# Kernel optimization log

Hardware: AMD Instinct MI355X
Metric: run time of the kernel (lower is better)

## Reference

```python
import jax, jax.numpy as jnp
import numpy as np

EDGE_TEXT_IMG = 2
D_MODEL = 256
N_HEADS = 8
N_LAYERS = 3
INPUT_DIM = 768
LN_EPS = 1e-5
CONFLICT_EPS = 1e-6


def setup_inputs() -> dict:
    key = jax.random.key(0)
    ks = jax.random.split(key, 32)
    B, N, E = 16, 512, 4096
    d, H, L = D_MODEL, N_HEADS, N_LAYERS
    s = 0.02
    inp = {
        'node_feats': jax.random.normal(ks[0], (B, N, INPUT_DIM), jnp.float32),
        'node_mask': jnp.ones((B, N), bool),
        'text_mask': jax.random.randint(ks[1], (B, N), 0, 2).astype(bool),
        'image_mask': jax.random.randint(ks[2], (B, N), 0, 2).astype(bool),
        'global_indices': jax.random.randint(ks[3], (B,), 0, N),
        'edge_index': jax.random.randint(ks[4], (B, 2, E), 0, N),
        'edge_type': jax.random.randint(ks[5], (B, E), 0, 4),
        'edge_weight': jax.random.uniform(ks[6], (B, E), jnp.float32),
        # params
        'W_in': jax.random.normal(ks[7], (INPUT_DIM, d)) * s,
        'b_in': jnp.zeros((d,)),
        'Wqkv': jax.random.normal(ks[8], (L, d, 3 * d)) * s,
        'bqkv': jnp.zeros((L, 3 * d)),
        'Wo': jax.random.normal(ks[9], (L, d, d)) * s,
        'bo': jnp.zeros((L, d)),
        'ln1_g': jnp.ones((L, d)), 'ln1_b': jnp.zeros((L, d)),
        'ln2_g': jnp.ones((L, d)), 'ln2_b': jnp.zeros((L, d)),
        'Wff1': jax.random.normal(ks[10], (L, d, 4 * d)) * s,
        'bff1': jnp.zeros((L, 4 * d)),
        'Wff2': jax.random.normal(ks[11], (L, 4 * d, d)) * s,
        'bff2': jnp.zeros((L, d)),
        'et_emb': jax.random.normal(ks[12], (4, H)) * s,
        'Wm1': jax.random.normal(ks[13], (3 * d + 1, 2 * d)) * s,
        'bm1': jnp.zeros((2 * d,)),
        'Wm2': jax.random.normal(ks[14], (2 * d, d)) * s,
        'bm2': jnp.zeros((d,)),
        'Wm3': jax.random.normal(ks[15], (d, 1)) * s,
        'bm3': jnp.zeros((1,)),
    }
    return inp


def _ln(x, g, b):
    mu = jnp.mean(x, -1, keepdims=True)
    var = jnp.mean((x - mu) ** 2, -1, keepdims=True)
    return (x - mu) * jax.lax.rsqrt(var + LN_EPS) * g + b


def _build_bias(edge_index, edge_type, edge_weight, et_emb, N):
    # vectorized scatter-add of per-edge head biases into dense [B,H,N,N]
    B = edge_index.shape[0]
    src, dst = edge_index[:, 0], edge_index[:, 1]  # [B,E]
    vals = et_emb[edge_type]  # [B,E,H]
    vals = vals + jnp.where(edge_type == EDGE_TEXT_IMG, edge_weight, 0.0)[..., None]
    bias = jnp.zeros((B, N, N, et_emb.shape[1]), vals.dtype)
    bias = bias.at[jnp.arange(B)[:, None], src, dst].add(vals)
    return bias.transpose(0, 3, 1, 2)  # [B,H,N,N]


def _forward(node_feats, node_mask, text_mask, image_mask, global_indices,
             edge_index, edge_type, edge_weight,
             W_in, b_in, Wqkv, bqkv, Wo, bo, ln1_g, ln1_b, ln2_g, ln2_b,
             Wff1, bff1, Wff2, bff2, et_emb, Wm1, bm1, Wm2, bm2, Wm3, bm3):
    B, N, _ = node_feats.shape
    H = N_HEADS
    hd = D_MODEL // H
    attn_bias = _build_bias(edge_index, edge_type, edge_weight, et_emb, N)
    x = node_feats @ W_in + b_in  # [B,N,d]
    key_mask = node_mask[:, None, None, :]  # [B,1,1,N]
    for l in range(N_LAYERS):
        qkv = x @ Wqkv[l] + bqkv[l]
        qkv = qkv.reshape(B, N, 3, H, hd).transpose(2, 0, 3, 1, 4)
        q, k, v = qkv[0], qkv[1], qkv[2]  # [B,H,N,hd]
        scores = jnp.einsum('bhnd,bhmd->bhnm', q, k) / np.sqrt(hd).astype(np.float32)
        scores = scores + attn_bias
        scores = jnp.where(key_mask, scores, -jnp.inf)
        attn = jax.nn.softmax(scores, axis=-1)
        out = jnp.einsum('bhnm,bhmd->bhnd', attn, v)
        out = out.transpose(0, 2, 1, 3).reshape(B, N, D_MODEL)
        out = out @ Wo[l] + bo[l]
        x = _ln(x + out, ln1_g[l], ln1_b[l])
        ff = jax.nn.gelu(x @ Wff1[l] + bff1[l], approximate=False) @ Wff2[l] + bff2[l]
        x = _ln(x + ff, ln2_g[l], ln2_b[l])
    tm = text_mask.astype(x.dtype)
    im = image_mask.astype(x.dtype)
    tc = jnp.clip(tm.sum(1, keepdims=True), 1.0)
    ic = jnp.clip(im.sum(1, keepdims=True), 1.0)
    text_pool = (x * tm[..., None]).sum(1) / tc
    image_pool = (x * im[..., None]).sum(1) / ic
    global_embeds = x[jnp.arange(B), global_indices]
    n1 = jnp.maximum(jnp.linalg.norm(text_pool, axis=-1), CONFLICT_EPS)
    n2 = jnp.maximum(jnp.linalg.norm(image_pool, axis=-1), CONFLICT_EPS)
    cos = jnp.sum(text_pool * image_pool, -1) / (n1 * n2)
    conflict = (1.0 - cos)[:, None]
    combined = jnp.concatenate([global_embeds, text_pool, image_pool, conflict], -1)
    h = jax.nn.gelu(combined @ Wm1 + bm1, approximate=False)
    h = jax.nn.gelu(h @ Wm2 + bm2, approximate=False)
    logits = (h @ Wm3 + bm3)[:, 0]
    return logits


def reference(node_feats, node_mask, text_mask, image_mask, global_indices,
              edge_index, edge_type, edge_weight,
              W_in, b_in, Wqkv, bqkv, Wo, bo, ln1_g, ln1_b, ln2_g, ln2_b,
              Wff1, bff1, Wff2, bff2, et_emb, Wm1, bm1, Wm2, bm2, Wm3, bm3):
    return _forward(node_feats, node_mask, text_mask, image_mask, global_indices,
                    edge_index, edge_type, edge_weight,
                    W_in, b_in, Wqkv, bqkv, Wo, bo, ln1_g, ln1_b, ln2_g, ln2_b,
                    Wff1, bff1, Wff2, bff2, et_emb, Wm1, bm1, Wm2, bm2, Wm3, bm3)
```

## Files before the change

kernel.cpp:

```cpp
#include <hip/hip_runtime.h>
#include <hip/hip_bf16.h>
#include <math.h>

#define Bb 16
#define Nn 512
#define Dd 256
#define Hh 8
#define HD 32
#define Ll 3
#define INDIM 768
#define Ee 4096
#define FF 1024
#define KP 40
#define NBUCK 32768

typedef unsigned short u16;
typedef __bf16 bf16x8 __attribute__((ext_vector_type(8)));
typedef float f32x4 __attribute__((ext_vector_type(4)));
typedef u16 us8 __attribute__((ext_vector_type(8)));
typedef u16 us4 __attribute__((ext_vector_type(4)));

__device__ __forceinline__ float gelu_exact(float x) {
    return 0.5f * x * (1.0f + erff(x * 0.70710678118654752f));
}

__device__ __forceinline__ u16 f2bf(float x) {
    unsigned int u = __float_as_uint(x);
    return (u16)((u + 0x7FFFu + ((u >> 16) & 1u)) >> 16);
}
__device__ __forceinline__ float bf2f(u16 h) {
    return __uint_as_float(((unsigned int)h) << 16);
}

__device__ __forceinline__ int ebucket(int b, int src, int dst) {
    return ((b * 32 + (src >> 4)) * 4 + (dst >> 7)) * 16 + (src & 15);
}


__global__ __launch_bounds__(256) void zero_kernel(int* __restrict__ p, int n) {
    int gid = blockIdx.x * 256 + threadIdx.x;
    if (gid < n) p[gid] = 0;
}

__global__ __launch_bounds__(256) void count_kernel(const int* __restrict__ edge_index,
                                                    int* __restrict__ counts) {
    int gid = blockIdx.x * 256 + threadIdx.x;
    int b = gid >> 12;
    int e = gid & (Ee - 1);
    int src = edge_index[b * 2 * Ee + e];
    int dst = edge_index[b * 2 * Ee + Ee + e];
    atomicAdd(&counts[ebucket(b, src, dst)], 1);
}

__global__ __launch_bounds__(1024) void scan_kernel(const int* __restrict__ counts,
                                                    int* __restrict__ offsets,
                                                    int* __restrict__ cursor) {
    __shared__ int ssum[1024];
    int t = threadIdx.x;
    int local[32];
    int s = 0;
#pragma unroll
    for (int i = 0; i < 32; i++) { local[i] = counts[t * 32 + i]; s += local[i]; }
    ssum[t] = s;
    __syncthreads();
    for (int off = 1; off < 1024; off *= 2) {
        __syncthreads();
        int v = (t >= off) ? ssum[t - off] : 0;
        __syncthreads();
        ssum[t] += v;
    }
    __syncthreads();
    int base = (t > 0) ? ssum[t - 1] : 0;
#pragma unroll
    for (int i = 0; i < 32; i++) {
        offsets[t * 32 + i] = base;
        cursor[t * 32 + i] = base;
        base += local[i];
    }
    if (t == 1023) offsets[NBUCK] = base;
}

__global__ __launch_bounds__(256) void scatter_kernel(const int* __restrict__ edge_index,
                                                      const int* __restrict__ edge_type,
                                                      const float* __restrict__ edge_weight,
                                                      int* __restrict__ cursor,
                                                      int2* __restrict__ pelist) {
    int gid = blockIdx.x * 256 + threadIdx.x;
    int b = gid >> 12;
    int e = gid & (Ee - 1);
    int src = edge_index[b * 2 * Ee + e];
    int dst = edge_index[b * 2 * Ee + Ee + e];
    int ty = edge_type[b * Ee + e];
    float wgt = edge_weight[b * Ee + e];
    int pos = atomicAdd(&cursor[ebucket(b, src, dst)], 1);
    int2 pe;
    pe.x = (src << 20) | (dst << 4) | ty;
    pe.y = __float_as_int(wgt);
    pelist[pos] = pe;
}


__global__ __launch_bounds__(256) void wsplit(const float* __restrict__ W,
                                              u16* __restrict__ Wh,
                                              u16* __restrict__ Wl,
                                              int K, int N) {
    size_t moff = (size_t)blockIdx.z * K * N;
    const float* Ws = W + moff;
    u16* Whs = Wh + moff;
    u16* Wls = Wl + moff;
    int n = blockIdx.x * 256 + threadIdx.x;
    int k0 = blockIdx.y * 8;
    float w[8];
#pragma unroll
    for (int i = 0; i < 8; i++) w[i] = Ws[(size_t)(k0 + i) * N + n];
    u16 h[8], l[8];
#pragma unroll
    for (int i = 0; i < 8; i++) {
        h[i] = f2bf(w[i]);
        l[i] = f2bf(w[i] - bf2f(h[i]));
    }
    us8 hv = {h[0], h[1], h[2], h[3], h[4], h[5], h[6], h[7]};
    us8 lv = {l[0], l[1], l[2], l[3], l[4], l[5], l[6], l[7]};
    *(us8*)&Whs[(size_t)n * K + k0] = hv;
    *(us8*)&Wls[(size_t)n * K + k0] = lv;
}


__global__ __launch_bounds__(256) void gemm_mfma64(const float* __restrict__ A,
                                                   const u16* __restrict__ Bh,
                                                   const u16* __restrict__ Bl,
                                                   const float* __restrict__ bias,
                                                   float* __restrict__ C,
                                                   int M, int K, int N, int act) {
    __shared__ u16 sAh[64 * KP];
    __shared__ u16 sAl[64 * KP];
    __shared__ u16 sBh[64 * KP];
    __shared__ u16 sBl[64 * KP];

    int t = threadIdx.x;
    int w = t >> 6, L = t & 63;
    int wr = w >> 1, wc = w & 1;
    int lane15 = L & 15, quad = L >> 4;
    int row0 = blockIdx.y * 64, col0 = blockIdx.x * 64;

    f32x4 acc[2][2];
#pragma unroll
    for (int mi = 0; mi < 2; mi++)
#pragma unroll
        for (int ni = 0; ni < 2; ni++) acc[mi][ni] = {0.f, 0.f, 0.f, 0.f};

    int ar0 = t >> 3, akq0 = (t & 7) * 4;
    int bn0 = t >> 2, bk0 = (t & 3) * 8;

    const float* Ap0 = &A[(size_t)(row0 + ar0) * K + akq0];
    const float* Ap1 = &A[(size_t)(row0 + ar0 + 32) * K + akq0];
    const u16* Bhp = &Bh[(size_t)(col0 + bn0) * K + bk0];
    const u16* Blp = &Bl[(size_t)(col0 + bn0) * K + bk0];

    float4 av0 = *(const float4*)&Ap0[0];
    float4 av1 = *(const float4*)&Ap1[0];
    us8 bhv = *(const us8*)&Bhp[0];
    us8 blv = *(const us8*)&Blp[0];

    for (int k0 = 0; k0 < K; k0 += 32) {
        __syncthreads();
        {
            float a[4] = {av0.x, av0.y, av0.z, av0.w};
            u16 h[4], l[4];
#pragma unroll
            for (int i = 0; i < 4; i++) { h[i] = f2bf(a[i]); l[i] = f2bf(a[i] - bf2f(h[i])); }
            us4 hv = {h[0], h[1], h[2], h[3]};
            us4 lv = {l[0], l[1], l[2], l[3]};
            *(us4*)&sAh[ar0 * KP + akq0] = hv;
            *(us4*)&sAl[ar0 * KP + akq0] = lv;
        }
        {
            float a[4] = {av1.x, av1.y, av1.z, av1.w};
            u16 h[4], l[4];
#pragma unroll
            for (int i = 0; i < 4; i++) { h[i] = f2bf(a[i]); l[i] = f2bf(a[i] - bf2f(h[i])); }
            us4 hv = {h[0], h[1], h[2], h[3]};
            us4 lv = {l[0], l[1], l[2], l[3]};
            *(us4*)&sAh[(ar0 + 32) * KP + akq0] = hv;
            *(us4*)&sAl[(ar0 + 32) * KP + akq0] = lv;
        }
        *(us8*)&sBh[bn0 * KP + bk0] = bhv;
        *(us8*)&sBl[bn0 * KP + bk0] = blv;
        __syncthreads();

        if (k0 + 32 < K) {
            av0 = *(const float4*)&Ap0[k0 + 32];
            av1 = *(const float4*)&Ap1[k0 + 32];
            bhv = *(const us8*)&Bhp[k0 + 32];
            blv = *(const us8*)&Blp[k0 + 32];
        }

        us8 ahr[2], alr[2], bhr[2], blr[2];
#pragma unroll
        for (int mi = 0; mi < 2; mi++) {
            int ro = (wr * 32 + mi * 16 + lane15) * KP + quad * 8;
            ahr[mi] = *(const us8*)&sAh[ro];
            alr[mi] = *(const us8*)&sAl[ro];
        }
#pragma unroll
        for (int ni = 0; ni < 2; ni++) {
            int ro = (wc * 32 + ni * 16 + lane15) * KP + quad * 8;
            bhr[ni] = *(const us8*)&sBh[ro];
            blr[ni] = *(const us8*)&sBl[ro];
        }
#pragma unroll
        for (int mi = 0; mi < 2; mi++) {
            bf16x8 ah = *(const bf16x8*)&ahr[mi];
            bf16x8 al = *(const bf16x8*)&alr[mi];
#pragma unroll
            for (int ni = 0; ni < 2; ni++) {
                bf16x8 bh = *(const bf16x8*)&bhr[ni];
                bf16x8 bl = *(const bf16x8*)&blr[ni];
                acc[mi][ni] = __builtin_amdgcn_mfma_f32_16x16x32_bf16(ah, bh, acc[mi][ni], 0, 0, 0);
                acc[mi][ni] = __builtin_amdgcn_mfma_f32_16x16x32_bf16(ah, bl, acc[mi][ni], 0, 0, 0);
                acc[mi][ni] = __builtin_amdgcn_mfma_f32_16x16x32_bf16(al, bh, acc[mi][ni], 0, 0, 0);
            }
        }
    }

#pragma unroll
    for (int mi = 0; mi < 2; mi++) {
#pragma unroll
        for (int ni = 0; ni < 2; ni++) {
            int col = col0 + wc * 32 + ni * 16 + lane15;
            float bcol = bias[col];
#pragma unroll
            for (int r = 0; r < 4; r++) {
                int row = row0 + wr * 32 + mi * 16 + quad * 4 + r;
                float u = acc[mi][ni][r] + bcol;
                if (act == 1) u = gelu_exact(u);
                C[(size_t)row * N + col] = u;
            }
        }
    }
}


__global__ __launch_bounds__(256) void gemm_mfma128(const float* __restrict__ A,
                                                    const u16* __restrict__ Bh,
                                                    const u16* __restrict__ Bl,
                                                    const float* __restrict__ bias,
                                                    float* __restrict__ C,
                                                    int M, int K, int N, int act) {
    __shared__ u16 sAh[128 * KP];
    __shared__ u16 sAl[128 * KP];
    __shared__ u16 sBh[128 * KP];
    __shared__ u16 sBl[128 * KP];

    int t = threadIdx.x;
    int w = t >> 6, L = t & 63;
    int wr = w >> 1, wc = w & 1;
    int lane15 = L & 15, quad = L >> 4;
    int row0 = blockIdx.y * 128, col0 = blockIdx.x * 128;

    f32x4 acc[4][4];
#pragma unroll
    for (int mi = 0; mi < 4; mi++)
#pragma unroll
        for (int ni = 0; ni < 4; ni++) acc[mi][ni] = {0.f, 0.f, 0.f, 0.f};

    int ar0 = t >> 3, ak0 = (t & 7) * 4;
    int bn0 = t >> 2, bk0 = (t & 3) * 8;

    const float* Ap = &A[(size_t)(row0 + ar0) * K + ak0];
    const u16* Bhp = &Bh[(size_t)(col0 + bn0) * K + bk0];
    const u16* Blp = &Bl[(size_t)(col0 + bn0) * K + bk0];

    float4 av[4];
    us8 bhv[2], blv[2];
#pragma unroll
    for (int i = 0; i < 4; i++) av[i] = *(const float4*)&Ap[(size_t)(32 * i) * K];
#pragma unroll
    for (int i = 0; i < 2; i++) {
        bhv[i] = *(const us8*)&Bhp[(size_t)(64 * i) * K];
        blv[i] = *(const us8*)&Blp[(size_t)(64 * i) * K];
    }

    for (int k0 = 0; k0 < K; k0 += 32) {
        __syncthreads();
#pragma unroll
        for (int i = 0; i < 4; i++) {
            float a[4] = {av[i].x, av[i].y, av[i].z, av[i].w};
            u16 h[4], l[4];
#pragma unroll
            for (int j = 0; j < 4; j++) { h[j] = f2bf(a[j]); l[j] = f2bf(a[j] - bf2f(h[j])); }
            us4 hv = {h[0], h[1], h[2], h[3]};
            us4 lv = {l[0], l[1], l[2], l[3]};
            *(us4*)&sAh[(ar0 + 32 * i) * KP + ak0] = hv;
            *(us4*)&sAl[(ar0 + 32 * i) * KP + ak0] = lv;
        }
#pragma unroll
        for (int i = 0; i < 2; i++) {
            *(us8*)&sBh[(bn0 + 64 * i) * KP + bk0] = bhv[i];
            *(us8*)&sBl[(bn0 + 64 * i) * KP + bk0] = blv[i];
        }
        __syncthreads();

        if (k0 + 32 < K) {
#pragma unroll
            for (int i = 0; i < 4; i++) av[i] = *(const float4*)&Ap[(size_t)(32 * i) * K + k0 + 32];
#pragma unroll
            for (int i = 0; i < 2; i++) {
                bhv[i] = *(const us8*)&Bhp[(size_t)(64 * i) * K + k0 + 32];
                blv[i] = *(const us8*)&Blp[(size_t)(64 * i) * K + k0 + 32];
            }
        }

        us8 ahr[4], alr[4], bhr[4], blr[4];
#pragma unroll
        for (int mi = 0; mi < 4; mi++) {
            int ro = (wr * 64 + mi * 16 + lane15) * KP + quad * 8;
            ahr[mi] = *(const us8*)&sAh[ro];
            alr[mi] = *(const us8*)&sAl[ro];
        }
#pragma unroll
        for (int ni = 0; ni < 4; ni++) {
            int ro = (wc * 64 + ni * 16 + lane15) * KP + quad * 8;
            bhr[ni] = *(const us8*)&sBh[ro];
            blr[ni] = *(const us8*)&sBl[ro];
        }
#pragma unroll
        for (int mi = 0; mi < 4; mi++) {
            bf16x8 ah = *(const bf16x8*)&ahr[mi];
            bf16x8 al = *(const bf16x8*)&alr[mi];
#pragma unroll
            for (int ni = 0; ni < 4; ni++) {
                bf16x8 bh = *(const bf16x8*)&bhr[ni];
                bf16x8 bl = *(const bf16x8*)&blr[ni];
                acc[mi][ni] = __builtin_amdgcn_mfma_f32_16x16x32_bf16(ah, bh, acc[mi][ni], 0, 0, 0);
                acc[mi][ni] = __builtin_amdgcn_mfma_f32_16x16x32_bf16(ah, bl, acc[mi][ni], 0, 0, 0);
                acc[mi][ni] = __builtin_amdgcn_mfma_f32_16x16x32_bf16(al, bh, acc[mi][ni], 0, 0, 0);
            }
        }
    }

#pragma unroll
    for (int mi = 0; mi < 4; mi++) {
#pragma unroll
        for (int ni = 0; ni < 4; ni++) {
            int col = col0 + wc * 64 + ni * 16 + lane15;
            float bcol = bias[col];
#pragma unroll
            for (int r = 0; r < 4; r++) {
                int row = row0 + wr * 64 + mi * 16 + quad * 4 + r;
                float u = acc[mi][ni][r] + bcol;
                if (act == 1) u = gelu_exact(u);
                C[(size_t)row * N + col] = u;
            }
        }
    }
}


#define SBP 132

__global__ __launch_bounds__(256, 2) void attn_kernel(const float* __restrict__ qkv,
                                                      const int* __restrict__ node_mask,
                                                      const int* __restrict__ offsets,
                                                      const int2* __restrict__ pelist,
                                                      const float* __restrict__ et_emb,
                                                      float* __restrict__ outbuf) {
    int bid = blockIdx.x;
    int quarter = bid & 3;
    int h = (bid >> 2) & 7;
    int b = bid >> 5;
    int t = threadIdx.x;
    int w = t >> 6, L = t & 63;
    int quad = L >> 4, lane15 = L & 15;
    int q8 = quad * 8;

    __shared__ u16 sKh[128 * 40];
    __shared__ u16 sKl[128 * 40];
    __shared__ u16 sVh[32 * SBP];
    __shared__ u16 sVl[32 * SBP];
    __shared__ float sS[4 * 16 * SBP];

    float* Sw = &sS[w * 16 * SBP];
    const float scale = 0.17677669529663687f;
    int nbase = quarter * 128 + w * 32;
    int mt0 = t >> 5, dt = t & 31;

    float etl0 = et_emb[0 * Hh + h];
    float etl1 = et_emb[1 * Hh + h];
    float etl2 = et_emb[2 * Hh + h];
    float etl3 = et_emb[3 * Hh + h];

    us8 Qh[2], Ql[2];
#pragma unroll
    for (int sub = 0; sub < 2; sub++) {
        size_t row = (size_t)(b * Nn + nbase + sub * 16 + lane15);
        float4 qa = *(const float4*)&qkv[row * 768 + h * HD + q8];
        float4 qb = *(const float4*)&qkv[row * 768 + h * HD + q8 + 4];
        float qv[8] = {qa.x, qa.y, qa.z, qa.w, qb.x, qb.y, qb.z, qb.w};
#pragma unroll
        for (int j = 0; j < 8; j++) {
            float xq = qv[j] * scale;
            u16 hh = f2bf(xq);
            Qh[sub][j] = hh;
            Ql[sub][j] = f2bf(xq - bf2f(hh));
        }
    }

    float Mst[2] = {-INFINITY, -INFINITY};
    float Lst[2] = {0.0f, 0.0f};
    f32x4 O[2][2];
#pragma unroll
    for (int sub = 0; sub < 2; sub++)
#pragma unroll
        for (int dc = 0; dc < 2; dc++) O[sub][dc] = {0.f, 0.f, 0.f, 0.f};

    float pk[16], pv[16];
#pragma unroll
    for (int j = 0; j < 16; j++) {
        size_t grow = (size_t)(b * Nn + mt0 + 8 * j) * 768 + h * HD + dt;
        pk[j] = qkv[grow + 256];
        pv[j] = qkv[grow + 512];
    }

    for (int T = 0; T < 4; T++) {
        int m0 = T * 128;
        __syncthreads();
#pragma unroll
        for (int j = 0; j < 16; j++) {
            int m = mt0 + 8 * j;
            u16 kh = f2bf(pk[j]);
            sKh[m * 40 + dt] = kh;
            sKl[m * 40 + dt] = f2bf(pk[j] - bf2f(kh));
            u16 vh = f2bf(pv[j]);
            sVh[dt * SBP + m] = vh;
            sVl[dt * SBP + m] = f2bf(pv[j] - bf2f(vh));
        }
        __syncthreads();
        if (T < 3) {
#pragma unroll
            for (int j = 0; j < 16; j++) {
                size_t grow = (size_t)(b * Nn + (T + 1) * 128 + mt0 + 8 * j) * 768 + h * HD + dt;
                pk[j] = qkv[grow + 256];
                pv[j] = qkv[grow + 512];
            }
        }

        float mk[4][8];
#pragma unroll
        for (int c = 0; c < 4; c++) {
            int4 u0 = *(const int4*)&node_mask[b * Nn + m0 + c * 32 + q8];
            int4 u1 = *(const int4*)&node_mask[b * Nn + m0 + c * 32 + q8 + 4];
            mk[c][0] = u0.x ? 0.f : -INFINITY;
            mk[c][1] = u0.y ? 0.f : -INFINITY;
            mk[c][2] = u0.z ? 0.f : -INFINITY;
            mk[c][3] = u0.w ? 0.f : -INFINITY;
            mk[c][4] = u1.x ? 0.f : -INFINITY;
            mk[c][5] = u1.y ? 0.f : -INFINITY;
            mk[c][6] = u1.z ? 0.f : -INFINITY;
            mk[c][7] = u1.w ? 0.f : -INFINITY;
        }

#pragma unroll
        for (int sub = 0; sub < 2; sub++) {
            int nsub = nbase + sub * 16;
            bf16x8 qh = *(const bf16x8*)&Qh[sub];
            bf16x8 ql = *(const bf16x8*)&Ql[sub];

            f32x4 accS[8];
#pragma unroll
            for (int mc = 0; mc < 8; mc++) accS[mc] = {0.f, 0.f, 0.f, 0.f};
#pragma unroll
            for (int mc = 0; mc < 8; mc++) {
                us8 khr = *(const us8*)&sKh[(mc * 16 + lane15) * 40 + q8];
                us8 klr = *(const us8*)&sKl[(mc * 16 + lane15) * 40 + q8];
                bf16x8 kh = *(const bf16x8*)&khr;
                bf16x8 kl = *(const bf16x8*)&klr;
                accS[mc] = __builtin_amdgcn_mfma_f32_16x16x32_bf16(qh, kh, accS[mc], 0, 0, 0);
                accS[mc] = __builtin_amdgcn_mfma_f32_16x16x32_bf16(qh, kl, accS[mc], 0, 0, 0);
                accS[mc] = __builtin_amdgcn_mfma_f32_16x16x32_bf16(ql, kh, accS[mc], 0, 0, 0);
            }
#pragma unroll
            for (int mc = 0; mc < 8; mc++)
#pragma unroll
                for (int r = 0; r < 4; r++)
                    Sw[(quad * 4 + r) * SBP + mc * 16 + lane15] = accS[mc][r];
            asm volatile("s_waitcnt lgkmcnt(0)" ::: "memory");

            int gb = ((b * 32 + (nsub >> 4)) * 4 + T) * 16;
            int beg = offsets[gb];
            int end = offsets[gb + 16];
            for (int i = beg + L; i < end; i += 64) {
                int2 pe = pelist[i];
                int sx = pe.x >> 20;
                int dx = (pe.x >> 4) & 511;
                int ty = pe.x & 3;
                float wgt = __int_as_float(pe.y);
                float val = (ty == 0) ? etl0 : (ty == 1) ? etl1 : (ty == 2) ? etl2 : etl3;
                if (ty == 2) val += wgt;
                atomicAdd(&Sw[(sx - nsub) * SBP + (dx - m0)], val);
            }
            asm volatile("s_waitcnt lgkmcnt(0)" ::: "memory");

            float s[4][8];
#pragma unroll
            for (int c = 0; c < 4; c++) {
                float4 a = *(const float4*)&Sw[lane15 * SBP + c * 32 + q8];
                float4 bq = *(const float4*)&Sw[lane15 * SBP + c * 32 + q8 + 4];
                s[c][0] = a.x + mk[c][0];  s[c][1] = a.y + mk[c][1];
                s[c][2] = a.z + mk[c][2];  s[c][3] = a.w + mk[c][3];
                s[c][4] = bq.x + mk[c][4]; s[c][5] = bq.y + mk[c][5];
                s[c][6] = bq.z + mk[c][6]; s[c][7] = bq.w + mk[c][7];
            }
            float mx = s[0][0];
#pragma unroll
            for (int c = 0; c < 4; c++)
#pragma unroll
                for (int j = 0; j < 8; j++) mx = fmaxf(mx, s[c][j]);
            mx = fmaxf(mx, __shfl_xor(mx, 16));
            mx = fmaxf(mx, __shfl_xor(mx, 32));
            float Mnew = fmaxf(Mst[sub], mx);
            float alpha = __expf(Mst[sub] - Mnew);
            float rs = 0.0f;
#pragma unroll
            for (int c = 0; c < 4; c++)
#pragma unroll
                for (int j = 0; j < 8; j++) {
                    s[c][j] = __expf(s[c][j] - Mnew);
                    rs += s[c][j];
                }
            rs += __shfl_xor(rs, 16);
            rs += __shfl_xor(rs, 32);
            Lst[sub] = Lst[sub] * alpha + rs;
            Mst[sub] = Mnew;

            us8 Ph[4], Pl[4];
#pragma unroll
            for (int c = 0; c < 4; c++)
#pragma unroll
                for (int j = 0; j < 8; j++) {
                    u16 ph = f2bf(s[c][j]);
                    Ph[c][j] = ph;
                    Pl[c][j] = f2bf(s[c][j] - bf2f(ph));
                }

            float aD[4];
#pragma unroll
            for (int r = 0; r < 4; r++) aD[r] = __shfl(alpha, (L & 48) | (quad * 4 + r));
#pragma unroll
            for (int dc = 0; dc < 2; dc++)
#pragma unroll
                for (int r = 0; r < 4; r++) O[sub][dc][r] *= aD[r];

#pragma unroll
            for (int c = 0; c < 4; c++) {
                bf16x8 ph = *(const bf16x8*)&Ph[c];
                bf16x8 pl = *(const bf16x8*)&Pl[c];
#pragma unroll
                for (int dc = 0; dc < 2; dc++) {
                    us8 vhr = *(const us8*)&sVh[(dc * 16 + lane15) * SBP + c * 32 + q8];
                    us8 vlr = *(const us8*)&sVl[(dc * 16 + lane15) * SBP + c * 32 + q8];
                    bf16x8 vh = *(const bf16x8*)&vhr;
                    bf16x8 vl = *(const bf16x8*)&vlr;
                    O[sub][dc] = __builtin_amdgcn_mfma_f32_16x16x32_bf16(ph, vh, O[sub][dc], 0, 0, 0);
                    O[sub][dc] = __builtin_amdgcn_mfma_f32_16x16x32_bf16(ph, vl, O[sub][dc], 0, 0, 0);
                    O[sub][dc] = __builtin_amdgcn_mfma_f32_16x16x32_bf16(pl, vh, O[sub][dc], 0, 0, 0);
                }
            }
        }
    }

#pragma unroll
    for (int sub = 0; sub < 2; sub++) {
        float linv = 1.0f / Lst[sub];
        float lD[4];
#pragma unroll
        for (int r = 0; r < 4; r++) lD[r] = __shfl(linv, (L & 48) | (quad * 4 + r));
#pragma unroll
        for (int dc = 0; dc < 2; dc++)
#pragma unroll
            for (int r = 0; r < 4; r++) {
                int row = nbase + sub * 16 + quad * 4 + r;
                outbuf[(size_t)(b * Nn + row) * Dd + h * HD + dc * 16 + lane15] =
                    O[sub][dc][r] * lD[r];
            }
    }
}


__global__ __launch_bounds__(256) void ln_kernel(float* __restrict__ x,
                                                 const float* __restrict__ res,
                                                 const float* __restrict__ g,
                                                 const float* __restrict__ bta) {
    int row = blockIdx.x;
    int t = threadIdx.x;
    __shared__ float red[4];
    __shared__ float stats[2];
    size_t idx = (size_t)row * Dd + t;
    float v = x[idx] + res[idx];
    float sm = v;
    for (int o = 32; o > 0; o >>= 1) sm += __shfl_down(sm, o);
    if ((t & 63) == 0) red[t >> 6] = sm;
    __syncthreads();
    if (t == 0) stats[0] = (red[0] + red[1] + red[2] + red[3]) * (1.0f / Dd);
    __syncthreads();
    float mu = stats[0];
    float dv = v - mu;
    float s2 = dv * dv;
    for (int o = 32; o > 0; o >>= 1) s2 += __shfl_down(s2, o);
    if ((t & 63) == 0) red[t >> 6] = s2;
    __syncthreads();
    if (t == 0) stats[1] = 1.0f / sqrtf((red[0] + red[1] + red[2] + red[3]) * (1.0f / Dd) + 1e-5f);
    __syncthreads();
    x[idx] = dv * stats[1] * g[t] + bta[t];
}


__global__ __launch_bounds__(256) void pool_kernel(const float* __restrict__ x,
                                                   const int* __restrict__ text_mask,
                                                   const int* __restrict__ image_mask,
                                                   float* __restrict__ pools) {
    int b = blockIdx.y;
    int n0 = blockIdx.x * 32;
    int t = threadIdx.x;
    float tp = 0.0f, ip = 0.0f, c1 = 0.0f, c2 = 0.0f;
    for (int n = n0; n < n0 + 32; n++) {
        float xv = x[(size_t)(b * Nn + n) * Dd + t];
        int tm = text_mask[b * Nn + n];
        int im = image_mask[b * Nn + n];
        tp += tm ? xv : 0.0f;
        ip += im ? xv : 0.0f;
        c1 += (float)tm;
        c2 += (float)im;
    }
    atomicAdd(&pools[b * 514 + t], tp);
    atomicAdd(&pools[b * 514 + 256 + t], ip);
    if (t == 0) {
        atomicAdd(&pools[b * 514 + 512], c1);
        atomicAdd(&pools[b * 514 + 513], c2);
    }
}

__global__ __launch_bounds__(256) void comb_kernel(const float* __restrict__ x,
                                                   const float* __restrict__ pools,
                                                   const int* __restrict__ gidx,
                                                   float* __restrict__ comb) {
    int b = blockIdx.x;
    int t = threadIdx.x;
    __shared__ float redd[12];
    float tc = fmaxf(pools[b * 514 + 512], 1.0f);
    float ic = fmaxf(pools[b * 514 + 513], 1.0f);
    float tp = pools[b * 514 + t] / tc;
    float ip = pools[b * 514 + 256 + t] / ic;
    int gi = gidx[b];
    comb[b * 776 + t] = x[(size_t)(b * Nn + gi) * Dd + t];
    comb[b * 776 + 256 + t] = tp;
    comb[b * 776 + 512 + t] = ip;
    float dotv = tp * ip, n1v = tp * tp, n2v = ip * ip;
    for (int o = 32; o > 0; o >>= 1) {
        dotv += __shfl_down(dotv, o);
        n1v += __shfl_down(n1v, o);
        n2v += __shfl_down(n2v, o);
    }
    if ((t & 63) == 0) { redd[t >> 6] = dotv; redd[4 + (t >> 6)] = n1v; redd[8 + (t >> 6)] = n2v; }
    __syncthreads();
    if (t == 0) {
        float dd = redd[0] + redd[1] + redd[2] + redd[3];
        float a1 = fmaxf(sqrtf(redd[4] + redd[5] + redd[6] + redd[7]), 1e-6f);
        float a2 = fmaxf(sqrtf(redd[8] + redd[9] + redd[10] + redd[11]), 1e-6f);
        comb[b * 776 + 768] = 1.0f - dd / (a1 * a2);
    }
}

__global__ __launch_bounds__(256) void h1_kernel(const float* __restrict__ comb,
                                                 const float* __restrict__ Wm1,
                                                 const float* __restrict__ bm1,
                                                 float* __restrict__ h1) {
    int b = blockIdx.y;
    int jc = blockIdx.x;
    int t = threadIdx.x;
    __shared__ float scomb[776];
    __shared__ float partial[2][128];
    for (int i = t; i < 769; i += 256) scomb[i] = comb[b * 776 + i];
    __syncthreads();
    int j = jc * 128 + (t & 127);
    int kh = t >> 7;
    int kbeg = kh ? 384 : 0;
    int kend = kh ? 769 : 384;
    float acc = 0.0f;
#pragma unroll 8
    for (int k = kbeg; k < kend; k++) acc += scomb[k] * Wm1[k * 512 + j];
    partial[kh][t & 127] = acc;
    __syncthreads();
    if (t < 128) {
        float v = partial[0][t] + partial[1][t] + bm1[jc * 128 + t];
        h1[b * 512 + jc * 128 + t] = gelu_exact(v);
    }
}

__global__ __launch_bounds__(256) void head_fin(const float* __restrict__ h1,
                                                const float* __restrict__ Wm2,
                                                const float* __restrict__ bm2,
                                                const float* __restrict__ Wm3,
                                                const float* __restrict__ bm3,
                                                float* __restrict__ out) {
    int b = blockIdx.x;
    int t = threadIdx.x;
    __shared__ float h1s[512];
    __shared__ float red[4];
    for (int i = t; i < 512; i += 256) h1s[i] = h1[b * 512 + i];
    __syncthreads();
    float acc = bm2[t];
#pragma unroll 8
    for (int k = 0; k < 512; k++) acc += h1s[k] * Wm2[k * 256 + t];
    float h2 = gelu_exact(acc);
    float lv = h2 * Wm3[t];
    for (int o = 32; o > 0; o >>= 1) lv += __shfl_down(lv, o);
    if ((t & 63) == 0) red[t >> 6] = lv;
    __syncthreads();
    if (t == 0) out[b] = red[0] + red[1] + red[2] + red[3] + bm3[0];
}


#define OFF_IN  0
#define OFF_QKV 196608
#define OFF_O   786432
#define OFF_F1  983040
#define OFF_F2  1769472
#define W_TOTAL 2555904

extern "C" void kernel_launch(void* const* d_in, const int* in_sizes, int n_in,
                              void* d_out, int out_size, void* d_ws, size_t ws_size,
                              hipStream_t stream) {
    const float* node_feats = (const float*)d_in[0];
    const int* node_mask = (const int*)d_in[1];
    const int* text_mask = (const int*)d_in[2];
    const int* image_mask = (const int*)d_in[3];
    const int* gidx = (const int*)d_in[4];
    const int* edge_index = (const int*)d_in[5];
    const int* edge_type = (const int*)d_in[6];
    const float* edge_weight = (const float*)d_in[7];
    const float* W_in = (const float*)d_in[8];
    const float* b_in = (const float*)d_in[9];
    const float* Wqkv = (const float*)d_in[10];
    const float* bqkv = (const float*)d_in[11];
    const float* Wo = (const float*)d_in[12];
    const float* bo = (const float*)d_in[13];
    const float* ln1_g = (const float*)d_in[14];
    const float* ln1_b = (const float*)d_in[15];
    const float* ln2_g = (const float*)d_in[16];
    const float* ln2_b = (const float*)d_in[17];
    const float* Wff1 = (const float*)d_in[18];
    const float* bff1 = (const float*)d_in[19];
    const float* Wff2 = (const float*)d_in[20];
    const float* bff2 = (const float*)d_in[21];
    const float* et_emb = (const float*)d_in[22];
    const float* Wm1 = (const float*)d_in[23];
    const float* bm1 = (const float*)d_in[24];
    const float* Wm2 = (const float*)d_in[25];
    const float* bm2 = (const float*)d_in[26];
    const float* Wm3 = (const float*)d_in[27];
    const float* bm3 = (const float*)d_in[28];

    const int M = Bb * Nn;
    char* ws = (char*)d_ws;
    size_t off = 0;
    auto alloc = [&](size_t bytes) {
        void* p = ws + off;
        off += (bytes + 255) & ~(size_t)255;
        return p;
    };
    float* x = (float*)alloc((size_t)M * Dd * 4);
    float* qkvb = (float*)alloc((size_t)M * FF * 4);
    float* ffb = qkvb;
    float* attnout = (float*)alloc((size_t)M * Dd * 4);
    float* projb = (float*)alloc((size_t)M * Dd * 4);
    int* counts = (int*)alloc((size_t)NBUCK * 4);
    int* offsets = (int*)alloc((size_t)(NBUCK + 1) * 4);
    int* cursor = (int*)alloc((size_t)NBUCK * 4);
    int2* pelist = (int2*)alloc((size_t)Bb * Ee * 8);
    float* pools = (float*)alloc((size_t)Bb * 514 * 4);
    float* comb = (float*)alloc((size_t)Bb * 776 * 4);
    float* h1 = (float*)alloc((size_t)Bb * 512 * 4);
    u16* wh = (u16*)alloc((size_t)W_TOTAL * 2);
    u16* wl = (u16*)alloc((size_t)W_TOTAL * 2);
    (void)ws_size;

    zero_kernel<<<NBUCK / 256, 256, 0, stream>>>(counts, NBUCK);
    zero_kernel<<<(Bb * 514 + 255) / 256, 256, 0, stream>>>((int*)pools, Bb * 514);
    count_kernel<<<256, 256, 0, stream>>>(edge_index, counts);
    scan_kernel<<<1, 1024, 0, stream>>>(counts, offsets, cursor);
    scatter_kernel<<<256, 256, 0, stream>>>(edge_index, edge_type, edge_weight, cursor, pelist);

    wsplit<<<dim3(1, 96, 1), 256, 0, stream>>>(W_in, wh + OFF_IN, wl + OFF_IN, 768, 256);
    wsplit<<<dim3(3, 32, 3), 256, 0, stream>>>(Wqkv, wh + OFF_QKV, wl + OFF_QKV, 256, 768);
    wsplit<<<dim3(1, 32, 3), 256, 0, stream>>>(Wo, wh + OFF_O, wl + OFF_O, 256, 256);
    wsplit<<<dim3(4, 32, 3), 256, 0, stream>>>(Wff1, wh + OFF_F1, wl + OFF_F1, 256, 1024);
    wsplit<<<dim3(1, 128, 3), 256, 0, stream>>>(Wff2, wh + OFF_F2, wl + OFF_F2, 1024, 256);

    gemm_mfma64<<<dim3(Dd / 64, M / 64), 256, 0, stream>>>(
        node_feats, wh + OFF_IN, wl + OFF_IN, b_in, x, M, INDIM, Dd, 0);

    for (int l = 0; l < Ll; l++) {
        gemm_mfma128<<<dim3(768 / 128, M / 128), 256, 0, stream>>>(
            x, wh + OFF_QKV + (size_t)l * 196608, wl + OFF_QKV + (size_t)l * 196608,
            bqkv + l * 768, qkvb, M, Dd, 768, 0);
        attn_kernel<<<Bb * Hh * 4, 256, 0, stream>>>(
            qkvb, node_mask, offsets, pelist, et_emb, attnout);
        gemm_mfma64<<<dim3(Dd / 64, M / 64), 256, 0, stream>>>(
            attnout, wh + OFF_O + (size_t)l * 65536, wl + OFF_O + (size_t)l * 65536,
            bo + l * Dd, projb, M, Dd, Dd, 0);
        ln_kernel<<<M, 256, 0, stream>>>(x, projb, ln1_g + l * Dd, ln1_b + l * Dd);
        gemm_mfma128<<<dim3(FF / 128, M / 128), 256, 0, stream>>>(
            x, wh + OFF_F1 + (size_t)l * 262144, wl + OFF_F1 + (size_t)l * 262144,
            bff1 + l * FF, ffb, M, Dd, FF, 1);
        gemm_mfma64<<<dim3(Dd / 64, M / 64), 256, 0, stream>>>(
            ffb, wh + OFF_F2 + (size_t)l * 262144, wl + OFF_F2 + (size_t)l * 262144,
            bff2 + l * Dd, projb, M, FF, Dd, 0);
        ln_kernel<<<M, 256, 0, stream>>>(x, projb, ln2_g + l * Dd, ln2_b + l * Dd);
    }

    pool_kernel<<<dim3(16, Bb), 256, 0, stream>>>(x, text_mask, image_mask, pools);
    comb_kernel<<<Bb, 256, 0, stream>>>(x, pools, gidx, comb);
    h1_kernel<<<dim3(4, Bb), 256, 0, stream>>>(comb, Wm1, bm1, h1);
    head_fin<<<Bb, 256, 0, stream>>>(h1, Wm2, bm2, Wm3, bm3, (float*)d_out);
}
```

Baseline: 660.2 us.

## Store intermediates as pre-split bf16 hi/lo pairs instead of fp32

```diff
diff --git a/kernel.cpp b/kernel.cpp
--- a/kernel.cpp
+++ b/kernel.cpp
@@ -126,12 +126,14 @@
 }
 
 
-__global__ __launch_bounds__(256) void gemm_mfma64(const float* __restrict__ A,
+__global__ __launch_bounds__(256) void gemm_f32a64(const float* __restrict__ A,
                                                    const u16* __restrict__ Bh,
                                                    const u16* __restrict__ Bl,
                                                    const float* __restrict__ bias,
-                                                   float* __restrict__ C,
-                                                   int M, int K, int N, int act) {
+                                                   float* __restrict__ Cf,
+                                                   u16* __restrict__ Ch,
+                                                   u16* __restrict__ Cl,
+                                                   int M, int K, int N, int mode) {
     __shared__ u16 sAh[64 * KP];
     __shared__ u16 sAl[64 * KP];
     __shared__ u16 sBh[64 * KP];
@@ -233,20 +235,134 @@
             for (int r = 0; r < 4; r++) {
                 int row = row0 + wr * 32 + mi * 16 + quad * 4 + r;
                 float u = acc[mi][ni][r] + bcol;
-                if (act == 1) u = gelu_exact(u);
-                C[(size_t)row * N + col] = u;
-            }
-        }
-    }
-}
-
-
-__global__ __launch_bounds__(256) void gemm_mfma128(const float* __restrict__ A,
-                                                    const u16* __restrict__ Bh,
-                                                    const u16* __restrict__ Bl,
-                                                    const float* __restrict__ bias,
-                                                    float* __restrict__ C,
-                                                    int M, int K, int N, int act) {
+                if (mode & 1) u = gelu_exact(u);
+                size_t idx = (size_t)row * N + col;
+                if (mode & 2) Cf[idx] = u;
+                if (mode & 4) {
+                    u16 hh = f2bf(u);
+                    Ch[idx] = hh;
+                    Cl[idx] = f2bf(u - bf2f(hh));
+                }
+            }
+        }
+    }
+}
+
+
+__global__ __launch_bounds__(256) void gemm_bf64(const u16* __restrict__ Ah,
+                                                 const u16* __restrict__ Al,
+                                                 const u16* __restrict__ Bh,
+                                                 const u16* __restrict__ Bl,
+                                                 const float* __restrict__ bias,
+                                                 float* __restrict__ Cf,
+                                                 u16* __restrict__ Ch,
+                                                 u16* __restrict__ Cl,
+                                                 int M, int K, int N, int mode) {
+    __shared__ u16 sAh[64 * KP];
+    __shared__ u16 sAl[64 * KP];
+    __shared__ u16 sBh[64 * KP];
+    __shared__ u16 sBl[64 * KP];
+
+    int t = threadIdx.x;
+    int w = t >> 6, L = t & 63;
+    int wr = w >> 1, wc = w & 1;
+    int lane15 = L & 15, quad = L >> 4;
+    int row0 = blockIdx.y * 64, col0 = blockIdx.x * 64;
+
+    f32x4 acc[2][2];
+#pragma unroll
+    for (int mi = 0; mi < 2; mi++)
+#pragma unroll
+        for (int ni = 0; ni < 2; ni++) acc[mi][ni] = {0.f, 0.f, 0.f, 0.f};
+
+    int r0 = t >> 2, kq = (t & 3) * 8;
+
+    const u16* Ahp = &Ah[(size_t)(row0 + r0) * K + kq];
+    const u16* Alp = &Al[(size_t)(row0 + r0) * K + kq];
+    const u16* Bhp = &Bh[(size_t)(col0 + r0) * K + kq];
+    const u16* Blp = &Bl[(size_t)(col0 + r0) * K + kq];
+
+    us8 ahv = *(const us8*)&Ahp[0];
+    us8 alv = *(const us8*)&Alp[0];
+    us8 bhv = *(const us8*)&Bhp[0];
+    us8 blv = *(const us8*)&Blp[0];
+
+    for (int k0 = 0; k0 < K; k0 += 32) {
+        __syncthreads();
+        *(us8*)&sAh[r0 * KP + kq] = ahv;
+        *(us8*)&sAl[r0 * KP + kq] = alv;
+        *(us8*)&sBh[r0 * KP + kq] = bhv;
+        *(us8*)&sBl[r0 * KP + kq] = blv;
+        __syncthreads();
+
+        if (k0 + 32 < K) {
+            ahv = *(const us8*)&Ahp[k0 + 32];
+            alv = *(const us8*)&Alp[k0 + 32];
+            bhv = *(const us8*)&Bhp[k0 + 32];
+            blv = *(const us8*)&Blp[k0 + 32];
+        }
+
+        us8 ahr[2], alr[2], bhr[2], blr[2];
+#pragma unroll
+        for (int mi = 0; mi < 2; mi++) {
+            int ro = (wr * 32 + mi * 16 + lane15) * KP + quad * 8;
+            ahr[mi] = *(const us8*)&sAh[ro];
+            alr[mi] = *(const us8*)&sAl[ro];
+        }
+#pragma unroll
+        for (int ni = 0; ni < 2; ni++) {
+            int ro = (wc * 32 + ni * 16 + lane15) * KP + quad * 8;
+            bhr[ni] = *(const us8*)&sBh[ro];
+            blr[ni] = *(const us8*)&sBl[ro];
+        }
+#pragma unroll
+        for (int mi = 0; mi < 2; mi++) {
+            bf16x8 ah = *(const bf16x8*)&ahr[mi];
+            bf16x8 al = *(const bf16x8*)&alr[mi];
+#pragma unroll
+            for (int ni = 0; ni < 2; ni++) {
+                bf16x8 bh = *(const bf16x8*)&bhr[ni];
+                bf16x8 bl = *(const bf16x8*)&blr[ni];
+                acc[mi][ni] = __builtin_amdgcn_mfma_f32_16x16x32_bf16(ah, bh, acc[mi][ni], 0, 0, 0);
+                acc[mi][ni] = __builtin_amdgcn_mfma_f32_16x16x32_bf16(ah, bl, acc[mi][ni], 0, 0, 0);
+                acc[mi][ni] = __builtin_amdgcn_mfma_f32_16x16x32_bf16(al, bh, acc[mi][ni], 0, 0, 0);
+            }
+        }
+    }
+
+#pragma unroll
+    for (int mi = 0; mi < 2; mi++) {
+#pragma unroll
+        for (int ni = 0; ni < 2; ni++) {
+            int col = col0 + wc * 32 + ni * 16 + lane15;
+            float bcol = bias[col];
+#pragma unroll
+            for (int r = 0; r < 4; r++) {
+                int row = row0 + wr * 32 + mi * 16 + quad * 4 + r;
+                float u = acc[mi][ni][r] + bcol;
+                if (mode & 1) u = gelu_exact(u);
+                size_t idx = (size_t)row * N + col;
+                if (mode & 2) Cf[idx] = u;
+                if (mode & 4) {
+                    u16 hh = f2bf(u);
+                    Ch[idx] = hh;
+                    Cl[idx] = f2bf(u - bf2f(hh));
+                }
+            }
+        }
+    }
+}
+
+
+__global__ __launch_bounds__(256) void gemm_bf128(const u16* __restrict__ Ah,
+                                                  const u16* __restrict__ Al,
+                                                  const u16* __restrict__ Bh,
+                                                  const u16* __restrict__ Bl,
+                                                  const float* __restrict__ bias,
+                                                  float* __restrict__ Cf,
+                                                  u16* __restrict__ Ch,
+                                                  u16* __restrict__ Cl,
+                                                  int M, int K, int N, int mode) {
     __shared__ u16 sAh[128 * KP];
     __shared__ u16 sAl[128 * KP];
     __shared__ u16 sBh[128 * KP];
@@ -264,19 +380,18 @@
 #pragma unroll
         for (int ni = 0; ni < 4; ni++) acc[mi][ni] = {0.f, 0.f, 0.f, 0.f};
 
-    int ar0 = t >> 3, ak0 = (t & 7) * 4;
-    int bn0 = t >> 2, bk0 = (t & 3) * 8;
-
-    const float* Ap = &A[(size_t)(row0 + ar0) * K + ak0];
-    const u16* Bhp = &Bh[(size_t)(col0 + bn0) * K + bk0];
-    const u16* Blp = &Bl[(size_t)(col0 + bn0) * K + bk0];
-
-    float4 av[4];
-    us8 bhv[2], blv[2];
-#pragma unroll
-    for (int i = 0; i < 4; i++) av[i] = *(const float4*)&Ap[(size_t)(32 * i) * K];
+    int r0 = t >> 2, kq = (t & 3) * 8;
+
+    const u16* Ahp = &Ah[(size_t)(row0 + r0) * K + kq];
+    const u16* Alp = &Al[(size_t)(row0 + r0) * K + kq];
+    const u16* Bhp = &Bh[(size_t)(col0 + r0) * K + kq];
+    const u16* Blp = &Bl[(size_t)(col0 + r0) * K + kq];
+
+    us8 ahv[2], alv[2], bhv[2], blv[2];
 #pragma unroll
     for (int i = 0; i < 2; i++) {
+        ahv[i] = *(const us8*)&Ahp[(size_t)(64 * i) * K];
+        alv[i] = *(const us8*)&Alp[(size_t)(64 * i) * K];
         bhv[i] = *(const us8*)&Bhp[(size_t)(64 * i) * K];
         blv[i] = *(const us8*)&Blp[(size_t)(64 * i) * K];
     }
@@ -284,28 +399,19 @@
     for (int k0 = 0; k0 < K; k0 += 32) {
         __syncthreads();
 #pragma unroll
-        for (int i = 0; i < 4; i++) {
-            float a[4] = {av[i].x, av[i].y, av[i].z, av[i].w};
-            u16 h[4], l[4];
-#pragma unroll
-            for (int j = 0; j < 4; j++) { h[j] = f2bf(a[j]); l[j] = f2bf(a[j] - bf2f(h[j])); }
-            us4 hv = {h[0], h[1], h[2], h[3]};
-            us4 lv = {l[0], l[1], l[2], l[3]};
-            *(us4*)&sAh[(ar0 + 32 * i) * KP + ak0] = hv;
-            *(us4*)&sAl[(ar0 + 32 * i) * KP + ak0] = lv;
-        }
-#pragma unroll
         for (int i = 0; i < 2; i++) {
-            *(us8*)&sBh[(bn0 + 64 * i) * KP + bk0] = bhv[i];
-            *(us8*)&sBl[(bn0 + 64 * i) * KP + bk0] = blv[i];
+            *(us8*)&sAh[(r0 + 64 * i) * KP + kq] = ahv[i];
+            *(us8*)&sAl[(r0 + 64 * i) * KP + kq] = alv[i];
+            *(us8*)&sBh[(r0 + 64 * i) * KP + kq] = bhv[i];
+            *(us8*)&sBl[(r0 + 64 * i) * KP + kq] = blv[i];
         }
         __syncthreads();
 
         if (k0 + 32 < K) {
 #pragma unroll
-            for (int i = 0; i < 4; i++) av[i] = *(const float4*)&Ap[(size_t)(32 * i) * K + k0 + 32];
-#pragma unroll
             for (int i = 0; i < 2; i++) {
+                ahv[i] = *(const us8*)&Ahp[(size_t)(64 * i) * K + k0 + 32];
+                alv[i] = *(const us8*)&Alp[(size_t)(64 * i) * K + k0 + 32];
                 bhv[i] = *(const us8*)&Bhp[(size_t)(64 * i) * K + k0 + 32];
                 blv[i] = *(const us8*)&Blp[(size_t)(64 * i) * K + k0 + 32];
             }
@@ -349,8 +455,14 @@
             for (int r = 0; r < 4; r++) {
                 int row = row0 + wr * 64 + mi * 16 + quad * 4 + r;
                 float u = acc[mi][ni][r] + bcol;
-                if (act == 1) u = gelu_exact(u);
-                C[(size_t)row * N + col] = u;
+                if (mode & 1) u = gelu_exact(u);
+                size_t idx = (size_t)row * N + col;
+                if (mode & 2) Cf[idx] = u;
+                if (mode & 4) {
+                    u16 hh = f2bf(u);
+                    Ch[idx] = hh;
+                    Cl[idx] = f2bf(u - bf2f(hh));
+                }
             }
         }
     }
@@ -359,12 +471,14 @@
 
 #define SBP 132
 
-__global__ __launch_bounds__(256, 2) void attn_kernel(const float* __restrict__ qkv,
+__global__ __launch_bounds__(256, 2) void attn_kernel(const u16* __restrict__ qkvh,
+                                                      const u16* __restrict__ qkvl,
                                                       const int* __restrict__ node_mask,
                                                       const int* __restrict__ offsets,
                                                       const int2* __restrict__ pelist,
                                                       const float* __restrict__ et_emb,
-                                                      float* __restrict__ outbuf) {
+                                                      u16* __restrict__ aoh,
+                                                      u16* __restrict__ aol) {
     int bid = blockIdx.x;
     int quarter = bid & 3;
     int h = (bid >> 2) & 7;
@@ -383,27 +497,19 @@
     float* Sw = &sS[w * 16 * SBP];
     const float scale = 0.17677669529663687f;
     int nbase = quarter * 128 + w * 32;
-    int mt0 = t >> 5, dt = t & 31;
+    int mt0 = t >> 3, d4 = (t & 7) * 4;
 
     float etl0 = et_emb[0 * Hh + h];
     float etl1 = et_emb[1 * Hh + h];
     float etl2 = et_emb[2 * Hh + h];
     float etl3 = et_emb[3 * Hh + h];
 
-    us8 Qh[2], Ql[2];
+    us8 Qhf[2], Qlf[2];
 #pragma unroll
     for (int sub = 0; sub < 2; sub++) {
         size_t row = (size_t)(b * Nn + nbase + sub * 16 + lane15);
-        float4 qa = *(const float4*)&qkv[row * 768 + h * HD + q8];
-        float4 qb = *(const float4*)&qkv[row * 768 + h * HD + q8 + 4];
-        float qv[8] = {qa.x, qa.y, qa.z, qa.w, qb.x, qb.y, qb.z, qb.w};
-#pragma unroll
-        for (int j = 0; j < 8; j++) {
-            float xq = qv[j] * scale;
-            u16 hh = f2bf(xq);
-            Qh[sub][j] = hh;
-            Ql[sub][j] = f2bf(xq - bf2f(hh));
-        }
+        Qhf[sub] = *(const us8*)&qkvh[row * 768 + h * HD + q8];
+        Qlf[sub] = *(const us8*)&qkvl[row * 768 + h * HD + q8];
     }
 
     float Mst[2] = {-INFINITY, -INFINITY};
@@ -414,34 +520,39 @@
 #pragma unroll
         for (int dc = 0; dc < 2; dc++) O[sub][dc] = {0.f, 0.f, 0.f, 0.f};
 
-    float pk[16], pv[16];
-#pragma unroll
-    for (int j = 0; j < 16; j++) {
-        size_t grow = (size_t)(b * Nn + mt0 + 8 * j) * 768 + h * HD + dt;
-        pk[j] = qkv[grow + 256];
-        pv[j] = qkv[grow + 512];
+    us4 pkh[4], pkl[4], pvh[4], pvl[4];
+#pragma unroll
+    for (int j = 0; j < 4; j++) {
+        size_t grow = (size_t)(b * Nn + mt0 + 32 * j) * 768 + h * HD + d4;
+        pkh[j] = *(const us4*)&qkvh[grow + 256];
+        pkl[j] = *(const us4*)&qkvl[grow + 256];
+        pvh[j] = *(const us4*)&qkvh[grow + 512];
+        pvl[j] = *(const us4*)&qkvl[grow + 512];
     }
 
     for (int T = 0; T < 4; T++) {
         int m0 = T * 128;
         __syncthreads();
 #pragma unroll
-        for (int j = 0; j < 16; j++) {
-            int m = mt0 + 8 * j;
-            u16 kh = f2bf(pk[j]);
-            sKh[m * 40 + dt] = kh;
-            sKl[m * 40 + dt] = f2bf(pk[j] - bf2f(kh));
-            u16 vh = f2bf(pv[j]);
-            sVh[dt * SBP + m] = vh;
-            sVl[dt * SBP + m] = f2bf(pv[j] - bf2f(vh));
+        for (int j = 0; j < 4; j++) {
+            int m = mt0 + 32 * j;
+            *(us4*)&sKh[m * 40 + d4] = pkh[j];
+            *(us4*)&sKl[m * 40 + d4] = pkl[j];
+#pragma unroll
+            for (int i = 0; i < 4; i++) {
+                sVh[(d4 + i) * SBP + m] = pvh[j][i];
+                sVl[(d4 + i) * SBP + m] = pvl[j][i];
+            }
         }
         __syncthreads();
         if (T < 3) {
 #pragma unroll
-            for (int j = 0; j < 16; j++) {
-                size_t grow = (size_t)(b * Nn + (T + 1) * 128 + mt0 + 8 * j) * 768 + h * HD + dt;
-                pk[j] = qkv[grow + 256];
-                pv[j] = qkv[grow + 512];
+            for (int j = 0; j < 4; j++) {
+                size_t grow = (size_t)(b * Nn + (T + 1) * 128 + mt0 + 32 * j) * 768 + h * HD + d4;
+                pkh[j] = *(const us4*)&qkvh[grow + 256];
+                pkl[j] = *(const us4*)&qkvl[grow + 256];
+                pvh[j] = *(const us4*)&qkvh[grow + 512];
+                pvl[j] = *(const us4*)&qkvl[grow + 512];
             }
         }
 
@@ -463,8 +574,8 @@
 #pragma unroll
         for (int sub = 0; sub < 2; sub++) {
             int nsub = nbase + sub * 16;
-            bf16x8 qh = *(const bf16x8*)&Qh[sub];
-            bf16x8 ql = *(const bf16x8*)&Ql[sub];
+            bf16x8 qfh = *(const bf16x8*)&Qhf[sub];
+            bf16x8 qfl = *(const bf16x8*)&Qlf[sub];
 
             f32x4 accS[8];
 #pragma unroll
@@ -475,15 +586,15 @@
                 us8 klr = *(const us8*)&sKl[(mc * 16 + lane15) * 40 + q8];
                 bf16x8 kh = *(const bf16x8*)&khr;
                 bf16x8 kl = *(const bf16x8*)&klr;
-                accS[mc] = __builtin_amdgcn_mfma_f32_16x16x32_bf16(qh, kh, accS[mc], 0, 0, 0);
-                accS[mc] = __builtin_amdgcn_mfma_f32_16x16x32_bf16(qh, kl, accS[mc], 0, 0, 0);
-                accS[mc] = __builtin_amdgcn_mfma_f32_16x16x32_bf16(ql, kh, accS[mc], 0, 0, 0);
+                accS[mc] = __builtin_amdgcn_mfma_f32_16x16x32_bf16(qfh, kh, accS[mc], 0, 0, 0);
+                accS[mc] = __builtin_amdgcn_mfma_f32_16x16x32_bf16(qfh, kl, accS[mc], 0, 0, 0);
+                accS[mc] = __builtin_amdgcn_mfma_f32_16x16x32_bf16(qfl, kh, accS[mc], 0, 0, 0);
             }
 #pragma unroll
             for (int mc = 0; mc < 8; mc++)
 #pragma unroll
                 for (int r = 0; r < 4; r++)
-                    Sw[(quad * 4 + r) * SBP + mc * 16 + lane15] = accS[mc][r];
+                    Sw[(quad * 4 + r) * SBP + mc * 16 + lane15] = accS[mc][r] * scale;
             asm volatile("s_waitcnt lgkmcnt(0)" ::: "memory");
 
             int gb = ((b * 32 + (nsub >> 4)) * 4 + T) * 16;
@@ -580,8 +691,11 @@
 #pragma unroll
             for (int r = 0; r < 4; r++) {
                 int row = nbase + sub * 16 + quad * 4 + r;
-                outbuf[(size_t)(b * Nn + row) * Dd + h * HD + dc * 16 + lane15] =
-                    O[sub][dc][r] * lD[r];
+                size_t idx = (size_t)(b * Nn + row) * Dd + h * HD + dc * 16 + lane15;
+                float o = O[sub][dc][r] * lD[r];
+                u16 hh = f2bf(o);
+                aoh[idx] = hh;
+                aol[idx] = f2bf(o - bf2f(hh));
             }
     }
 }
@@ -590,7 +704,9 @@
 __global__ __launch_bounds__(256) void ln_kernel(float* __restrict__ x,
                                                  const float* __restrict__ res,
                                                  const float* __restrict__ g,
-                                                 const float* __restrict__ bta) {
+                                                 const float* __restrict__ bta,
+                                                 u16* __restrict__ xh,
+                                                 u16* __restrict__ xl) {
     int row = blockIdx.x;
     int t = threadIdx.x;
     __shared__ float red[4];
@@ -611,7 +727,11 @@
     __syncthreads();
     if (t == 0) stats[1] = 1.0f / sqrtf((red[0] + red[1] + red[2] + red[3]) * (1.0f / Dd) + 1e-5f);
     __syncthreads();
-    x[idx] = dv * stats[1] * g[t] + bta[t];
+    float out = dv * stats[1] * g[t] + bta[t];
+    x[idx] = out;
+    u16 hh = f2bf(out);
+    xh[idx] = hh;
+    xl[idx] = f2bf(out - bf2f(hh));
 }
 
 
@@ -770,9 +890,14 @@
         return p;
     };
     float* x = (float*)alloc((size_t)M * Dd * 4);
-    float* qkvb = (float*)alloc((size_t)M * FF * 4);
-    float* ffb = qkvb;
-    float* attnout = (float*)alloc((size_t)M * Dd * 4);
+    u16* xh = (u16*)alloc((size_t)M * Dd * 2);
+    u16* xl = (u16*)alloc((size_t)M * Dd * 2);
+    u16* qkvh = (u16*)alloc((size_t)M * 768 * 2);
+    u16* qkvl = (u16*)alloc((size_t)M * 768 * 2);
+    u16* aoh = (u16*)alloc((size_t)M * Dd * 2);
+    u16* aol = (u16*)alloc((size_t)M * Dd * 2);
+    u16* f1h = (u16*)alloc((size_t)M * FF * 2);
+    u16* f1l = (u16*)alloc((size_t)M * FF * 2);
     float* projb = (float*)alloc((size_t)M * Dd * 4);
     int* counts = (int*)alloc((size_t)NBUCK * 4);
     int* offsets = (int*)alloc((size_t)(NBUCK + 1) * 4);
@@ -797,26 +922,26 @@
     wsplit<<<dim3(4, 32, 3), 256, 0, stream>>>(Wff1, wh + OFF_F1, wl + OFF_F1, 256, 1024);
     wsplit<<<dim3(1, 128, 3), 256, 0, stream>>>(Wff2, wh + OFF_F2, wl + OFF_F2, 1024, 256);
 
-    gemm_mfma64<<<dim3(Dd / 64, M / 64), 256, 0, stream>>>(
-        node_feats, wh + OFF_IN, wl + OFF_IN, b_in, x, M, INDIM, Dd, 0);
+    gemm_f32a64<<<dim3(Dd / 64, M / 64), 256, 0, stream>>>(
+        node_feats, wh + OFF_IN, wl + OFF_IN, b_in, x, xh, xl, M, INDIM, Dd, 2 | 4);
 
     for (int l = 0; l < Ll; l++) {
-        gemm_mfma128<<<dim3(768 / 128, M / 128), 256, 0, stream>>>(
-            x, wh + OFF_QKV + (size_t)l * 196608, wl + OFF_QKV + (size_t)l * 196608,
-            bqkv + l * 768, qkvb, M, Dd, 768, 0);
+        gemm_bf128<<<dim3(768 / 128, M / 128), 256, 0, stream>>>(
+            xh, xl, wh + OFF_QKV + (size_t)l * 196608, wl + OFF_QKV + (size_t)l * 196608,
+            bqkv + l * 768, nullptr, qkvh, qkvl, M, Dd, 768, 4);
         attn_kernel<<<Bb * Hh * 4, 256, 0, stream>>>(
-            qkvb, node_mask, offsets, pelist, et_emb, attnout);
-        gemm_mfma64<<<dim3(Dd / 64, M / 64), 256, 0, stream>>>(
-            attnout, wh + OFF_O + (size_t)l * 65536, wl + OFF_O + (size_t)l * 65536,
-            bo + l * Dd, projb, M, Dd, Dd, 0);
-        ln_kernel<<<M, 256, 0, stream>>>(x, projb, ln1_g + l * Dd, ln1_b + l * Dd);
-        gemm_mfma128<<<dim3(FF / 128, M / 128), 256, 0, stream>>>(
-            x, wh + OFF_F1 + (size_t)l * 262144, wl + OFF_F1 + (size_t)l * 262144,
-            bff1 + l * FF, ffb, M, Dd, FF, 1);
-        gemm_mfma64<<<dim3(Dd / 64, M / 64), 256, 0, stream>>>(
-            ffb, wh + OFF_F2 + (size_t)l * 262144, wl + OFF_F2 + (size_t)l * 262144,
-            bff2 + l * Dd, projb, M, FF, Dd, 0);
-        ln_kernel<<<M, 256, 0, stream>>>(x, projb, ln2_g + l * Dd, ln2_b + l * Dd);
+            qkvh, qkvl, node_mask, offsets, pelist, et_emb, aoh, aol);
+        gemm_bf64<<<dim3(Dd / 64, M / 64), 256, 0, stream>>>(
+            aoh, aol, wh + OFF_O + (size_t)l * 65536, wl + OFF_O + (size_t)l * 65536,
+            bo + l * Dd, projb, nullptr, nullptr, M, Dd, Dd, 2);
+        ln_kernel<<<M, 256, 0, stream>>>(x, projb, ln1_g + l * Dd, ln1_b + l * Dd, xh, xl);
+        gemm_bf128<<<dim3(FF / 128, M / 128), 256, 0, stream>>>(
+            xh, xl, wh + OFF_F1 + (size_t)l * 262144, wl + OFF_F1 + (size_t)l * 262144,
+            bff1 + l * FF, nullptr, f1h, f1l, M, Dd, FF, 1 | 4);
+        gemm_bf64<<<dim3(Dd / 64, M / 64), 256, 0, stream>>>(
+            f1h, f1l, wh + OFF_F2 + (size_t)l * 262144, wl + OFF_F2 + (size_t)l * 262144,
+            bff2 + l * Dd, projb, nullptr, nullptr, M, FF, Dd, 2);
+        ln_kernel<<<M, 256, 0, stream>>>(x, projb, ln2_g + l * Dd, ln2_b + l * Dd, xh, xl);
     }
 
     pool_kernel<<<dim3(16, Bb), 256, 0, stream>>>(x, text_mask, image_mask, pools);
```

Result: slower. 709.9 us (+7.5%).
